# Performance work log

Measured on AMD Instinct MI355X. Metric: run time of the kernel, lower is better.

The kernel has to match this reference:

```python
import jax, jax.numpy as jnp
from jax import lax
import numpy as np

BN_EPS = 1e-3  # ultralytics BatchNorm2d default eps

def setup_inputs() -> dict:
    key = jax.random.key(0)
    ks = jax.random.split(key, 6)
    B, C, H, W = 16, 64, 160, 160
    E, R = 4, 16  # experts, reduced router dim = C // reduction
    return {
        "x": jax.random.normal(ks[0], (B, C, H, W), jnp.float32),
        "fc1_w": jax.random.normal(ks[1], (R, C), jnp.float32) * 0.1,
        "fc2_w": jax.random.normal(ks[2], (E, R), jnp.float32) * 0.1,
        "fc2_b": jax.random.normal(ks[3], (E,), jnp.float32) * 0.1,
        "conv_w": jax.random.normal(ks[4], (E, C, C, 3, 3), jnp.float32) * 0.05,
        "bn_gamma": jnp.ones((E, C), jnp.float32),
        "bn_beta": jnp.zeros((E, C), jnp.float32),
        "bn_mean": jax.random.normal(ks[5], (E, C), jnp.float32) * 0.1,
        "bn_var": jnp.ones((E, C), jnp.float32),
    }

def reference(x, fc1_w, fc2_w, fc2_b, conv_w, bn_gamma, bn_beta, bn_mean, bn_var):
    # Router: global avg pool -> fc1 -> relu -> fc2 -> softmax over experts
    g = jnp.mean(x, axis=(2, 3))                       # [B, C]
    h = jax.nn.relu(g @ fc1_w.T)                       # [B, R]
    w = jax.nn.softmax(h @ fc2_w.T + fc2_b, axis=1)    # [B, E]

    def expert(kernel, gamma, beta, mean, var):
        # Conv2d(bias=False, pad=k//2) + BatchNorm2d (eval) + SiLU
        y = lax.conv_general_dilated(
            x, kernel, window_strides=(1, 1), padding="SAME",
            dimension_numbers=("NCHW", "OIHW", "NCHW"))
        scale = (gamma * lax.rsqrt(var + BN_EPS))[None, :, None, None]
        shift = (beta - mean * gamma * lax.rsqrt(var + BN_EPS))[None, :, None, None]
        return jax.nn.silu(y * scale + shift)          # [B, Co, H, W]

    outs = jax.vmap(expert)(conv_w, bn_gamma, bn_beta, bn_mean, bn_var)  # [E, B, Co, H, W]
    return jnp.einsum("ebchw,be->bchw", outs, w)
```

## Files before the change

### kernel.cpp

```cpp
#include <hip/hip_runtime.h>
#include <hip/hip_bf16.h>

typedef unsigned short u16;
typedef unsigned int   u32;
typedef __attribute__((ext_vector_type(8))) short s16x8;
typedef __attribute__((ext_vector_type(16))) float f32x16;

#define BN_EPS 1e-3f
#define NB 16
#define NC 64
#define NH 160
#define NW 160
#define HP 162
#define WPD 162

#define OFF_XT 0UL
#define SZ_XT  (16UL*162*162*64*2)
#define OFF_WT (OFF_XT + SZ_XT)
#define SZ_WT  (4UL*64*9*64*2)
#define OFF_SH (OFF_WT + SZ_WT)
#define OFF_G  (OFF_SH + 1024UL)
#define OFF_WE (OFF_G + 4096UL)
#define OFF_GP (OFF_WE + 256UL)

#define XSTRIDE 342
#define XLS_BYTES (8 * XSTRIDE * 16)
#define WLS_BYTES (2304 * 16)
#define SMEM_TOTAL (XLS_BYTES + WLS_BYTES)

__device__ __forceinline__ u16 f2bf(float f) {
    u32 u = __builtin_bit_cast(u32, f);
    u += 0x7fffu + ((u >> 16) & 1u);
    return (u16)(u >> 16);
}

__global__ void prep_w(const float* __restrict__ cw, u16* __restrict__ wt,
                       const float* __restrict__ gamma, const float* __restrict__ beta,
                       const float* __restrict__ mean, const float* __restrict__ var,
                       float* __restrict__ shift) {
    int idx = blockIdx.x * 256 + threadIdx.x;
    if (idx < 4 * 2 * 9 * 4 * 64 * 8) {
        int cin = idx & 7;
        int t = idx >> 3;
        int co = t & 63; t >>= 6;
        int cio = t & 3; t >>= 2;
        int pos = t % 9; t /= 9;
        int ch = t & 1;
        int e = t >> 1;
        int tsp = (pos % 3) * 3 + (pos / 3);
        int ci = ch * 32 + cio * 8 + cin;
        int ec = e * 64 + co;
        float sc = gamma[ec] * rsqrtf(var[ec] + BN_EPS);
        wt[idx] = f2bf(cw[(((long)ec) * 64 + ci) * 9 + tsp] * sc);
    }
    if (idx < 256) {
        float sc = gamma[idx] * rsqrtf(var[idx] + BN_EPS);
        shift[idx] = beta[idx] - mean[idx] * sc;
    }
}

__global__ void prep_x(const float* __restrict__ x, u16* __restrict__ xt,
                       float* __restrict__ gpart) {
    __shared__ float tile[64][33];
    int blk = blockIdx.x;
    int t = threadIdx.x;
    if (blk >= 12800) {
        int bb = blk - 12800;
        int hp = bb % 162, b = bb / 162;
        u32* row = (u32*)xt + (((long)b * 162 + hp) * 162) * 32;
        if (hp == 0 || hp == 161) {
            for (int i = t; i < 162 * 32; i += 256) row[i] = 0u;
        } else if (t < 64) {
            int p = (t >> 5) ? 161 : 0;
            row[p * 32 + (t & 31)] = 0u;
        }
        return;
    }
    int wt5 = blk % 5;
    int tmp = blk / 5;
    int h = tmp % 160, b = tmp / 160;
    int w0 = wt5 * 32;
    int w = t & 31, c0 = t >> 5;
#pragma unroll
    for (int i = 0; i < 8; ++i) {
        int c = c0 + 8 * i;
        tile[c][w] = x[(((long)b * 64 + c) * 160 + h) * 160 + w0 + w];
    }
    __syncthreads();
    if (t < 64) {
        float s = 0.f;
#pragma unroll
        for (int wi = 0; wi < 32; ++wi) s += tile[t][wi];
        gpart[((long)(b * 64 + t)) * 800 + h * 5 + wt5] = s;
    }
    u32* xt32 = (u32*)xt;
    long base = ((((long)b * 162 + h + 1) * 162) + (w0 + 1)) * 32;
#pragma unroll
    for (int j = 0; j < 4; ++j) {
        int idx = t + 256 * j;
        int p = idx >> 5, cp = idx & 31;
        float v0 = tile[2 * cp][p], v1 = tile[2 * cp + 1][p];
        xt32[base + p * 32 + cp] = (u32)f2bf(v0) | ((u32)f2bf(v1) << 16);
    }
}

__global__ void g_reduce(const float* __restrict__ gpart, float* __restrict__ g) {
    int id = blockIdx.x;
    int t = threadIdx.x;
    float s = 0.f;
    for (int i = t; i < 800; i += 256) s += gpart[(long)id * 800 + i];
#pragma unroll
    for (int off = 32; off > 0; off >>= 1) s += __shfl_down(s, off, 64);
    __shared__ float red[4];
    if ((t & 63) == 0) red[t >> 6] = s;
    __syncthreads();
    if (t == 0) g[id] = (red[0] + red[1] + red[2] + red[3]) * (1.f / 25600.f);
}

__global__ void router(const float* __restrict__ g, const float* __restrict__ fc1w,
                       const float* __restrict__ fc2w, const float* __restrict__ fc2b,
                       float* __restrict__ wexp) {
    __shared__ float gL[16][64];
    __shared__ float h1[16][16];
    __shared__ float z[16][4];
    int t = threadIdx.x;
    for (int i = t; i < 1024; i += 256) gL[i >> 6][i & 63] = g[i];
    __syncthreads();
    {
        int b = t >> 4, r = t & 15;
        float s = 0.f;
#pragma unroll
        for (int c = 0; c < 64; ++c) s += gL[b][c] * fc1w[r * 64 + c];
        h1[b][r] = fmaxf(s, 0.f);
    }
    __syncthreads();
    if (t < 64) {
        int b = t >> 2, e = t & 3;
        float s = fc2b[e];
#pragma unroll
        for (int r = 0; r < 16; ++r) s += h1[b][r] * fc2w[e * 16 + r];
        z[b][e] = s;
    }
    __syncthreads();
    if (t < 16) {
        int b = t;
        float m = fmaxf(fmaxf(z[b][0], z[b][1]), fmaxf(z[b][2], z[b][3]));
        float e0 = __expf(z[b][0] - m), e1 = __expf(z[b][1] - m);
        float e2 = __expf(z[b][2] - m), e3 = __expf(z[b][3] - m);
        float inv = 1.f / (e0 + e1 + e2 + e3);
        wexp[b * 4 + 0] = e0 * inv; wexp[b * 4 + 1] = e1 * inv;
        wexp[b * 4 + 2] = e2 * inv; wexp[b * 4 + 3] = e3 * inv;
    }
}

__global__ __launch_bounds__(256, 2) void conv_main(
    const u16* __restrict__ xt, const u16* __restrict__ wt,
    const float* __restrict__ shift,
    const float* __restrict__ wexp, float* __restrict__ out) {
    extern __shared__ char smem[];
    u16* xls = (u16*)smem;
    u16* wls = (u16*)(smem + XLS_BYTES);

    const int o = blockIdx.x;
    const int blk = (o & 7) * 200 + (o >> 3);
    const int wt5 = blk % 5;
    const int tmp = blk / 5;
    const int ht = tmp % 20;
    const int b = tmp / 20;
    const int h0 = ht * 8, w0 = wt5 * 32;
    const int tid = threadIdx.x;
    const int lane = tid & 63;
    const int wv = tid >> 6;
    const int l31 = lane & 31, kh = lane >> 5;
    const int r0 = 2 * wv;

    {
#pragma unroll
        for (int r = 0; r < 9; ++r) {
            int oo = r * 256 + tid;
            __builtin_amdgcn_global_load_lds(
                (const __attribute__((address_space(1))) void*)(wt + oo * 8),
                (__attribute__((address_space(3))) void*)(wls + oo * 8),
                16, 0, 0);
        }
    }
    {
        const u16* xb = xt + (long)b * HP * WPD * 64;
        for (int c = tid; c < 2720; c += 256) {
            int P = c >> 3, cg = c & 7;
            int y = P / 34, px = P - y * 34;
            const u16* src = xb + (((long)(h0 + y) * WPD) + (w0 + px)) * 64 + cg * 8;
            s16x8 v = *(const s16x8*)src;
            *(s16x8*)(&xls[(cg * XSTRIDE + P) << 3]) = v;
        }
    }

    const int oA2 = (kh * 64 + l31) << 3;
    const int oBk0 = ((kh * XSTRIDE) + r0 * 34 + l31) << 3;
    const int oBk1 = oBk0 + ((2 * XSTRIDE) << 3);

    f32x16 acc00 = (f32x16)(0.f), acc01 = (f32x16)(0.f);
    f32x16 acc10 = (f32x16)(0.f), acc11 = (f32x16)(0.f);
    f32x16 oac00 = (f32x16)(0.f), oac01 = (f32x16)(0.f);
    f32x16 oac10 = (f32x16)(0.f), oac11 = (f32x16)(0.f);

    auto epi = [&](int E) {
        const float we = wexp[(b << 2) + E];
        const float* shE = shift + (E << 6);
#pragma unroll
        for (int j = 0; j < 16; ++j) {
            const int cob = (j & 3) + 8 * (j >> 2) + 4 * kh;
            {
                float sh = shE[cob];
                float y0 = acc00[j] + sh;
                float y1 = acc01[j] + sh;
                oac00[j] += we * (y0 * __builtin_amdgcn_rcpf(1.f + __expf(-y0)));
                oac01[j] += we * (y1 * __builtin_amdgcn_rcpf(1.f + __expf(-y1)));
            }
            {
                float sh = shE[cob + 32];
                float y0 = acc10[j] + sh;
                float y1 = acc11[j] + sh;
                oac10[j] += we * (y0 * __builtin_amdgcn_rcpf(1.f + __expf(-y0)));
                oac11[j] += we * (y1 * __builtin_amdgcn_rcpf(1.f + __expf(-y1)));
            }
        }
        acc00 = (f32x16)(0.f); acc01 = (f32x16)(0.f);
        acc10 = (f32x16)(0.f); acc11 = (f32x16)(0.f);
    };

#pragma unroll 1
    for (int s = 0; s < 8; ++s) {
        const int ch = s & 1;
        if (s > 0) {
            __syncthreads();
            const u16* wsrc = wt + ((long)s) * 2304 * 8;
#pragma unroll
            for (int r = 0; r < 9; ++r) {
                int oo = r * 256 + tid;
                __builtin_amdgcn_global_load_lds(
                    (const __attribute__((address_space(1))) void*)(wsrc + oo * 8),
                    (__attribute__((address_space(3))) void*)(wls + oo * 8),
                    16, 0, 0);
            }
        }
        const int chU = (ch * 4 * XSTRIDE) << 3;
        const int b0U = oBk0 + chU;
        const int b1U = oBk1 + chU;

        auto dx_group = [&](int g, int pos0) {
            const int gU = g << 3;
            s16x8 B00 = *(const s16x8*)(&xls[b0U + gU]);
            s16x8 B01 = *(const s16x8*)(&xls[b1U + gU]);
            s16x8 B10 = *(const s16x8*)(&xls[b0U + gU + (34 << 3)]);
            s16x8 B11 = *(const s16x8*)(&xls[b1U + gU + (34 << 3)]);
            s16x8 B20 = *(const s16x8*)(&xls[b0U + gU + (68 << 3)]);
            s16x8 B21 = *(const s16x8*)(&xls[b1U + gU + (68 << 3)]);
            s16x8 B30 = *(const s16x8*)(&xls[b0U + gU + (102 << 3)]);
            s16x8 B31 = *(const s16x8*)(&xls[b1U + gU + (102 << 3)]);
            __builtin_amdgcn_s_setprio(1);
#pragma unroll
            for (int dy = 0; dy < 3; ++dy) {
                const int atU = oA2 + (pos0 + dy) * 2048;
                s16x8 a00 = *(const s16x8*)(&wls[atU]);
                s16x8 a10 = *(const s16x8*)(&wls[atU + 256]);
                s16x8 a01 = *(const s16x8*)(&wls[atU + 1024]);
                s16x8 a11 = *(const s16x8*)(&wls[atU + 1280]);
                s16x8 bn00 = (dy == 0) ? B00 : (dy == 1) ? B10 : B20;
                s16x8 bn01 = (dy == 0) ? B01 : (dy == 1) ? B11 : B21;
                s16x8 bn10 = (dy == 0) ? B10 : (dy == 1) ? B20 : B30;
                s16x8 bn11 = (dy == 0) ? B11 : (dy == 1) ? B21 : B31;
                acc00 = __builtin_amdgcn_mfma_f32_32x32x16_bf16(a00, bn00, acc00, 0, 0, 0);
                acc10 = __builtin_amdgcn_mfma_f32_32x32x16_bf16(a10, bn00, acc10, 0, 0, 0);
                acc01 = __builtin_amdgcn_mfma_f32_32x32x16_bf16(a00, bn10, acc01, 0, 0, 0);
                acc11 = __builtin_amdgcn_mfma_f32_32x32x16_bf16(a10, bn10, acc11, 0, 0, 0);
                acc00 = __builtin_amdgcn_mfma_f32_32x32x16_bf16(a01, bn01, acc00, 0, 0, 0);
                acc10 = __builtin_amdgcn_mfma_f32_32x32x16_bf16(a11, bn01, acc10, 0, 0, 0);
                acc01 = __builtin_amdgcn_mfma_f32_32x32x16_bf16(a01, bn11, acc01, 0, 0, 0);
                acc11 = __builtin_amdgcn_mfma_f32_32x32x16_bf16(a11, bn11, acc11, 0, 0, 0);
            }
            __builtin_amdgcn_s_setprio(0);
        };

        if (s == 0) __builtin_amdgcn_s_waitcnt(0x070);
        else        __builtin_amdgcn_s_waitcnt(0xF76);
        __builtin_amdgcn_s_barrier();
        __builtin_amdgcn_sched_barrier(0);
        dx_group(0, 0);

        __builtin_amdgcn_s_waitcnt(0xF73);
        __builtin_amdgcn_s_barrier();
        __builtin_amdgcn_sched_barrier(0);
        dx_group(1, 3);

        __builtin_amdgcn_s_waitcnt(0xF70);
        __builtin_amdgcn_s_barrier();
        __builtin_amdgcn_sched_barrier(0);
        dx_group(2, 6);

        if (ch == 1) epi(s >> 1);
    }

    const int yy = h0 + r0;
#pragma unroll
    for (int j = 0; j < 16; ++j) {
        const int cob = (j & 3) + 8 * (j >> 2) + 4 * kh;
        out[(((long)(b * 64 + cob)) * 160 + yy) * 160 + w0 + l31] = oac00[j];
        out[(((long)(b * 64 + cob)) * 160 + yy + 1) * 160 + w0 + l31] = oac01[j];
        out[(((long)(b * 64 + cob + 32)) * 160 + yy) * 160 + w0 + l31] = oac10[j];
        out[(((long)(b * 64 + cob + 32)) * 160 + yy + 1) * 160 + w0 + l31] = oac11[j];
    }
}

extern "C" void kernel_launch(void* const* d_in, const int* in_sizes, int n_in,
                              void* d_out, int out_size, void* d_ws, size_t ws_size,
                              hipStream_t stream) {
    const float* x = (const float*)d_in[0];
    const float* fc1w = (const float*)d_in[1];
    const float* fc2w = (const float*)d_in[2];
    const float* fc2b = (const float*)d_in[3];
    const float* convw = (const float*)d_in[4];
    const float* gamma = (const float*)d_in[5];
    const float* beta = (const float*)d_in[6];
    const float* mean = (const float*)d_in[7];
    const float* var = (const float*)d_in[8];
    float* out = (float*)d_out;
    char* ws = (char*)d_ws;
    u16* xt = (u16*)(ws + OFF_XT);
    u16* wtb = (u16*)(ws + OFF_WT);
    float* shift = (float*)(ws + OFF_SH);
    float* g = (float*)(ws + OFF_G);
    float* wexp = (float*)(ws + OFF_WE);
    float* gpart = (float*)(ws + OFF_GP);

    hipFuncSetAttribute((const void*)conv_main,
                        hipFuncAttributeMaxDynamicSharedMemorySize, SMEM_TOTAL);

    prep_w<<<576, 256, 0, stream>>>(convw, wtb, gamma, beta, mean, var, shift);
    prep_x<<<15392, 256, 0, stream>>>(x, xt, gpart);
    g_reduce<<<1024, 256, 0, stream>>>(gpart, g);
    router<<<1, 256, 0, stream>>>(g, fc1w, fc2w, fc2b, wexp);
    conv_main<<<1600, 256, SMEM_TOTAL, stream>>>(xt, wtb, shift, wexp, out);
}
```

Before: 180.1 us.

## Prefetch next weight chunk during current compute and cache shift and router weights

Issues the global-to-LDS load for the next step's weights early instead of waiting for a full sync at the top of each step. The first six rows load after groups 0-1 finish using them, and the last three load after group 2, so the transfer overlaps with compute. It also copies BN shifts into LDS and hoists the per-expert routing weights into registers. This adds waitcnt and barrier reasoning that is easy to get wrong, and may add LDS pressure.

```diff
diff --git a/kernel.cpp b/kernel.cpp
--- a/kernel.cpp
+++ b/kernel.cpp
@@ -26,7 +26,8 @@
 #define XSTRIDE 342
 #define XLS_BYTES (8 * XSTRIDE * 16)
 #define WLS_BYTES (2304 * 16)
-#define SMEM_TOTAL (XLS_BYTES + WLS_BYTES)
+#define SHLS_BYTES 1024
+#define SMEM_TOTAL (XLS_BYTES + WLS_BYTES + SHLS_BYTES)
 
 __device__ __forceinline__ u16 f2bf(float f) {
     u32 u = __builtin_bit_cast(u32, f);
@@ -160,6 +161,7 @@
     extern __shared__ char smem[];
     u16* xls = (u16*)smem;
     u16* wls = (u16*)(smem + XLS_BYTES);
+    float* shls = (float*)(smem + XLS_BYTES + WLS_BYTES);
 
     const int o = blockIdx.x;
     const int blk = (o & 7) * 200 + (o >> 3);
@@ -184,6 +186,11 @@
                 16, 0, 0);
         }
     }
+    const float we0 = wexp[(b << 2) + 0];
+    const float we1 = wexp[(b << 2) + 1];
+    const float we2 = wexp[(b << 2) + 2];
+    const float we3 = wexp[(b << 2) + 3];
+    shls[tid] = shift[tid];
     {
         const u16* xb = xt + (long)b * HP * WPD * 64;
         for (int c = tid; c < 2720; c += 256) {
@@ -205,8 +212,8 @@
     f32x16 oac10 = (f32x16)(0.f), oac11 = (f32x16)(0.f);
 
     auto epi = [&](int E) {
-        const float we = wexp[(b << 2) + E];
-        const float* shE = shift + (E << 6);
+        const float we = (E == 0) ? we0 : (E == 1) ? we1 : (E == 2) ? we2 : we3;
+        const float* shE = shls + (E << 6);
 #pragma unroll
         for (int j = 0; j < 16; ++j) {
             const int cob = (j & 3) + 8 * (j >> 2) + 4 * kh;
@@ -232,18 +239,6 @@
 #pragma unroll 1
     for (int s = 0; s < 8; ++s) {
         const int ch = s & 1;
-        if (s > 0) {
-            __syncthreads();
-            const u16* wsrc = wt + ((long)s) * 2304 * 8;
-#pragma unroll
-            for (int r = 0; r < 9; ++r) {
-                int oo = r * 256 + tid;
-                __builtin_amdgcn_global_load_lds(
-                    (const __attribute__((address_space(1))) void*)(wsrc + oo * 8),
-                    (__attribute__((address_space(3))) void*)(wls + oo * 8),
-                    16, 0, 0);
-            }
-        }
         const int chU = (ch * 4 * XSTRIDE) << 3;
         const int b0U = oBk0 + chU;
         const int b1U = oBk1 + chU;
@@ -283,22 +278,42 @@
         };
 
         if (s == 0) __builtin_amdgcn_s_waitcnt(0x070);
-        else        __builtin_amdgcn_s_waitcnt(0xF76);
+        else        __builtin_amdgcn_s_waitcnt(0xF73);
         __builtin_amdgcn_s_barrier();
         __builtin_amdgcn_sched_barrier(0);
         dx_group(0, 0);
-
-        __builtin_amdgcn_s_waitcnt(0xF73);
-        __builtin_amdgcn_s_barrier();
-        __builtin_amdgcn_sched_barrier(0);
         dx_group(1, 3);
 
         __builtin_amdgcn_s_waitcnt(0xF70);
         __builtin_amdgcn_s_barrier();
         __builtin_amdgcn_sched_barrier(0);
+        if (s < 7) {
+            const u16* wsrc = wt + ((long)(s + 1)) * 2304 * 8;
+#pragma unroll
+            for (int r = 0; r < 6; ++r) {
+                int oo = r * 256 + tid;
+                __builtin_amdgcn_global_load_lds(
+                    (const __attribute__((address_space(1))) void*)(wsrc + oo * 8),
+                    (__attribute__((address_space(3))) void*)(wls + oo * 8),
+                    16, 0, 0);
+            }
+        }
         dx_group(2, 6);
-
         if (ch == 1) epi(s >> 1);
+
+        __builtin_amdgcn_s_barrier();
+        __builtin_amdgcn_sched_barrier(0);
+        if (s < 7) {
+            const u16* wsrc = wt + ((long)(s + 1)) * 2304 * 8;
+#pragma unroll
+            for (int r = 6; r < 9; ++r) {
+                int oo = r * 256 + tid;
+                __builtin_amdgcn_global_load_lds(
+                    (const __attribute__((address_space(1))) void*)(wsrc + oo * 8),
+                    (__attribute__((address_space(3))) void*)(wls + oo * 8),
+                    16, 0, 0);
+            }
+        }
     }
 
     const int yy = h0 + r0;
```

Result: no change. 178.4 us (-0.9%).
